# Kernel optimization log

Hardware: AMD Instinct MI355X
Metric: run time of the kernel (lower is better)

## Reference

```python
import jax, jax.numpy as jnp
import numpy as np

B, KVH, HPK, D = 4, 8, 4, 128          # batch, n_kv_heads, n_heads_per_kv, head_size
SEQ_KV = 4096                           # cached history length
SEQ = SEQ_KV + 1                        # history + current token
K, LOCAL_K, SINK, RANK = 512, 128, 4, 32


def gather(t, axis, i):
    """Broadcasting take_along_axis, mirroring the torch `gather` helper."""
    axis = axis % t.ndim
    tgt = list(t.shape)
    tgt[axis] = i.shape[axis]
    return jnp.take_along_axis(t, jnp.broadcast_to(i, tgt), axis)


def sparse_q_score(q, key_cpu_t, cur_key_t):
    # q: (B,KVH,HPK,1,D); key_cpu_t: (B,KVH,D,SEQ_KV); cur_key_t: (B,KVH,1,D,1)
    absq = jnp.abs(q).sum(2, keepdims=True)                    # (B,KVH,1,1,D)
    _, idx = jax.lax.top_k(absq, RANK)                         # (B,KVH,1,1,RANK)
    q_proj = gather(q, -1, idx)                                # (B,KVH,HPK,1,RANK)
    idx_t = jnp.swapaxes(idx, -1, -2)                          # (B,KVH,1,RANK,1)
    k_hist = gather(key_cpu_t[:, :, None], -2, idx_t)          # (B,KVH,1,RANK,SEQ_KV)
    k_cur = gather(cur_key_t, -2, idx_t)                       # (B,KVH,1,RANK,1)
    k_proj = jnp.concatenate([k_hist, k_cur], -1)              # (B,KVH,1,RANK,SEQ)
    scale = jnp.sqrt(jnp.abs(q_proj).sum(-1) / jnp.abs(q).sum(-1) * D)[..., None]
    return jnp.matmul(q_proj, k_proj) / scale                  # (B,KVH,HPK,1,SEQ)


def setup_inputs():
    key = jax.random.key(0)
    ks = jax.random.split(key, 6)
    query = jax.random.normal(ks[0], (B, KVH * HPK, 1, D), jnp.float32)
    k = jax.random.normal(ks[1], (B, KVH, 1, D), jnp.float32)
    v = jax.random.normal(ks[2], (B, KVH, 1, D), jnp.float32)
    logmask = jnp.zeros((B, KVH * HPK, 1, SEQ), jnp.float32)
    key_cpu = jax.random.normal(ks[3], (B, KVH, SEQ_KV, D), jnp.float32)
    value_cpu = jax.random.normal(ks[4], (B, KVH, SEQ_KV, D), jnp.float32)
    s_key_cpu = jnp.swapaxes(key_cpu, -1, -2)                  # head-size-contiguous copy
    mean_v = jax.random.normal(ks[5], (B, KVH, 1, 1, D), jnp.float32)
    return {"query": query, "key": k, "value": v, "logmask": logmask,
            "key_cpu": key_cpu, "value_cpu": value_cpu,
            "s_key_cpu": s_key_cpu, "mean_v": mean_v}


def reference(query, key, value, logmask, key_cpu, value_cpu, s_key_cpu, mean_v):
    q = query.reshape(B, KVH, HPK, 1, D)
    k = key.reshape(B, KVH, 1, 1, D)
    v = value.reshape(B, KVH, 1, 1, D)
    lm = logmask.reshape(B, KVH, HPK, 1, SEQ)
    # approximate scores over the full key history + current key
    score = (sparse_q_score(q, s_key_cpu, jnp.swapaxes(k, 3, 4)) + lm).astype(jnp.float32)
    # causal index over history (excluding current token): 0 = most recent unmasked
    neg = jnp.isneginf(lm[..., :-1])
    ci = jnp.where(neg, -1,
                   jnp.cumsum((~neg)[..., ::-1].astype(jnp.int32), -1)[..., ::-1] - 1)
    is_local = (0 <= ci) & (ci < LOCAL_K)
    is_sink = ci >= SEQ - SINK - 1
    fmax = jnp.finfo(jnp.float32).max
    topk_score = jnp.where(is_local | is_sink, fmax, score[..., :-1]).sum(2, keepdims=True)
    kk = min(K + SINK, SEQ)
    _, indices = jax.lax.top_k(topk_score, kk)                 # (B,KVH,1,1,kk)
    # running mean value update
    mean_v_new = (mean_v * (SEQ - 1) + v.astype(jnp.float32)) / SEQ
    # weight reallocation to the mean value
    norm = jax.nn.softmax(score, -1)
    kv_weight = gather(norm, -1, indices).sum(-1) + norm[..., -1]  # (B,KVH,HPK,1)
    # gather selected K/V and append current token
    kv_idx = indices[..., 0, :, None]                          # (B,KVH,1,kk,1)
    key_g = jnp.concatenate([gather(key_cpu[:, :, None], -2, kv_idx), k], -2)   # (B,KVH,1,kk+1,D)
    val_g = jnp.concatenate([gather(value_cpu[:, :, None], -2, kv_idx), v], -2)
    cur_idx = jnp.full(indices.shape[:-1] + (1,), SEQ - 1, indices.dtype)
    lm_g = gather(lm, -1, jnp.concatenate([indices, cur_idx], -1))  # (B,KVH,HPK,1,kk+1)
    # dense attention over the reduced key set
    scores = jnp.matmul(q, jnp.swapaxes(key_g, -1, -2)) * (D ** -0.5) + lm_g
    weights = jax.nn.softmax(scores.astype(jnp.float32), -1) * kv_weight[..., None]
    out = jnp.matmul(weights, val_g) + (1.0 - kv_weight[..., None]) * mean_v_new
    return out.reshape(B, KVH * HPK, 1, D), weights.reshape(B, KVH * HPK, 1, kk + 1)
```

## Files before the change

### kernel.cpp

```cpp
#include <hip/hip_runtime.h>
#include <hip/hip_bf16.h>
#include <math.h>

#define NBH 32
#define HPKN 4
#define DN 128
#define SEQKV 4096
#define SEQN 4097
#define SSTR 4100
#define RANKN 32
#define KSEL 516
#define SINKN 4
#define LOCALK 128
#define NMASK 132
#define NTOP 384
#define NCHUNK 16

__global__ __launch_bounds__(256) void k2_scores(
    const float* __restrict__ q, const float* __restrict__ key,
    const float* __restrict__ skey, const float* __restrict__ lm,
    float* __restrict__ scores, float* __restrict__ tk,
    float2* __restrict__ partials) {
  int bh = blockIdx.y;
  int s0 = blockIdx.x << 8;
  int t = threadIdx.x;
  int wave = t >> 6, lane = t & 63;
  __shared__ float qv[4][128];
  __shared__ float absq[128];
  __shared__ int sel[RANKN];
  __shared__ float qp[4][RANKN];
  __shared__ float wred[4][4];

  {
    float v0 = q[(size_t)bh * 512 + t];
    float v1 = q[(size_t)bh * 512 + 256 + t];
    qv[t >> 7][t & 127] = v0;
    qv[2 + (t >> 7)][t & 127] = v1;
  }
  __syncthreads();
  if (t < 128)
    absq[t] = fabsf(qv[0][t]) + fabsf(qv[1][t]) + fabsf(qv[2][t]) + fabsf(qv[3][t]);
  __syncthreads();
  if (t < 128) {
    float a = absq[t];
    int rank = 0;
    for (int e = 0; e < 128; ++e) {
      float ae = absq[e];
      rank += (ae > a) || (ae == a && e < t);
    }
    if (rank < RANKN) sel[rank] = t;
  }
  __syncthreads();
  {
    float fa = fabsf(qv[wave][lane]) + fabsf(qv[wave][lane + 64]);
    for (int off = 32; off > 0; off >>= 1) fa += __shfl_down(fa, off);
    float full = __shfl(fa, 0);
    float qsel = (lane < RANKN) ? qv[wave][sel[lane]] : 0.f;
    float sv = fabsf(qsel);
    for (int off = 32; off > 0; off >>= 1) sv += __shfl_down(sv, off);
    float selsum = __shfl(sv, 0);
    float scale = sqrtf(selsum / full * 128.f);
    if (lane < RANKN) qp[wave][lane] = qsel / scale;
  }
  __syncthreads();

  if (blockIdx.x == 0) {
    float kv = (lane < RANKN) ? key[bh * 128 + sel[lane]] : 0.f;
    float pr = (lane < RANKN) ? qp[wave][lane] * kv : 0.f;
    for (int off = 32; off > 0; off >>= 1) pr += __shfl_down(pr, off);
    if (lane == 0)
      scores[(size_t)(bh * 4 + wave) * SSTR + SEQKV] =
          pr + lm[(size_t)(bh * 4 + wave) * SEQN + SEQKV];
  }

  const float* kb = skey + (size_t)bh * 128 * 4096;
  float a0 = 0, a1 = 0, a2 = 0, a3 = 0;
#pragma unroll 8
  for (int r = 0; r < RANKN; ++r) {
    float k0 = kb[((size_t)sel[r] << 12) + s0 + t];
    a0 += qp[0][r] * k0;
    a1 += qp[1][r] * k0;
    a2 += qp[2][r] * k0;
    a3 += qp[3][r] * k0;
  }
  float sc[4];
  {
    int s = s0 + t;
    sc[0] = a0 + lm[(size_t)(bh * 4 + 0) * SEQN + s];
    sc[1] = a1 + lm[(size_t)(bh * 4 + 1) * SEQN + s];
    sc[2] = a2 + lm[(size_t)(bh * 4 + 2) * SEQN + s];
    sc[3] = a3 + lm[(size_t)(bh * 4 + 3) * SEQN + s];
    float sum = sc[0] + sc[1] + sc[2] + sc[3];
#pragma unroll
    for (int p = 0; p < 4; ++p)
      scores[(size_t)(bh * 4 + p) * SSTR + s] = sc[p];
    tk[(bh << 12) + s] = sum;
  }

#pragma unroll
  for (int p = 0; p < 4; ++p) {
    float mx = sc[p];
    for (int off = 32; off > 0; off >>= 1) mx = fmaxf(mx, __shfl_down(mx, off));
    if (lane == 0) wred[wave][p] = mx;
  }
  __syncthreads();
  float bm[4];
#pragma unroll
  for (int p = 0; p < 4; ++p)
    bm[p] = fmaxf(fmaxf(wred[0][p], wred[1][p]), fmaxf(wred[2][p], wred[3][p]));
  __syncthreads();
#pragma unroll
  for (int p = 0; p < 4; ++p) {
    float e = expf(sc[p] - bm[p]);
    for (int off = 32; off > 0; off >>= 1) e += __shfl_down(e, off);
    if (lane == 0) wred[wave][p] = e;
  }
  __syncthreads();
  if (t < 4) {
    float s = wred[0][t] + wred[1][t] + wred[2][t] + wred[3][t];
    partials[(size_t)(bh * 4 + t) * NCHUNK + blockIdx.x] = make_float2(bm[t], s);
  }
}

__global__ __launch_bounds__(256) void k3_topk(
    const float* __restrict__ tk, int* __restrict__ indices) {
  int bh = blockIdx.x;
  int t = threadIdx.x;
  int lane = t & 63;
  __shared__ unsigned us[4096];
  __shared__ unsigned hist[2048];
  __shared__ unsigned long long binlist[2048];
  __shared__ unsigned long long selk[512];
  __shared__ unsigned chunkSum[32];
  __shared__ int c1, c2, binB_s, nAbove_s, needed_s;

  {
    const float4* tk4 = (const float4*)(tk + (bh << 12));
    for (int i = t; i < 1024; i += 256) {
      float4 v = tk4[i];
      unsigned b0 = __float_as_uint(v.x), b1 = __float_as_uint(v.y);
      unsigned b2 = __float_as_uint(v.z), b3 = __float_as_uint(v.w);
      us[i * 4 + 0] = (b0 & 0x80000000u) ? ~b0 : (b0 | 0x80000000u);
      us[i * 4 + 1] = (b1 & 0x80000000u) ? ~b1 : (b1 | 0x80000000u);
      us[i * 4 + 2] = (b2 & 0x80000000u) ? ~b2 : (b2 | 0x80000000u);
      us[i * 4 + 3] = (b3 & 0x80000000u) ? ~b3 : (b3 | 0x80000000u);
    }
  }
  for (int i = t; i < 2048; i += 256) hist[i] = 0;
  if (t == 0) { c1 = 0; c2 = 0; }
  __syncthreads();

  for (int s = SINKN + t; s < SEQKV - LOCALK; s += 256)
    atomicAdd(&hist[us[s] >> 21], 1u);
  __syncthreads();

  if (t < 32) {
    unsigned sum = 0;
    for (int i = 0; i < 64; ++i) sum += hist[t * 64 + i];
    chunkSum[t] = sum;
  }
  __syncthreads();

  if (t < 64) {
    int l = t;
    unsigned x = (l < 32) ? chunkSum[l] : 0;
    unsigned sfx = x;
    for (int off = 1; off < 64; off <<= 1) {
      unsigned y = __shfl_down(sfx, off);
      if (l + off < 64) sfx += y;
    }
    unsigned above = sfx - x;
    bool hit = (l < 32) && (above < NTOP) && (above + x >= NTOP);
    unsigned long long mask = __ballot(hit);
    int C = __ffsll(mask) - 1;
    unsigned aboveC = __shfl(above, C);
    unsigned h = hist[C * 64 + l];
    unsigned sfx2 = h;
    for (int off = 1; off < 64; off <<= 1) {
      unsigned y = __shfl_down(sfx2, off);
      if (l + off < 64) sfx2 += y;
    }
    unsigned above2 = aboveC + (sfx2 - h);
    bool hit2 = (above2 < NTOP) && (above2 + h >= NTOP);
    unsigned long long mask2 = __ballot(hit2);
    int lB = __ffsll(mask2) - 1;
    if (l == lB) {
      binB_s = C * 64 + l;
      nAbove_s = (int)above2;
      needed_s = NTOP - (int)above2;
    }
  }
  __syncthreads();
  unsigned B = (unsigned)binB_s;
  int nAbove = nAbove_s, needed = needed_s;

  for (int s0 = SINKN; s0 < SEQKV - LOCALK; s0 += 256) {
    int s = s0 + t;
    bool valid = (s < SEQKV - LOCALK);
    unsigned u = valid ? us[s] : 0u;
    unsigned bin = u >> 21;
    bool win = valid && (bin > B);
    bool bnd = valid && (bin == B);
    unsigned long long mw = __ballot(win);
    unsigned long long mb = __ballot(bnd);
    int bw = 0, bb = 0;
    if (lane == 0) {
      if (mw) bw = atomicAdd(&c1, __popcll(mw));
      if (mb) bb = atomicAdd(&c2, __popcll(mb));
    }
    bw = __shfl(bw, 0);
    bb = __shfl(bb, 0);
    unsigned long long lmask = (1ULL << lane) - 1ULL;
    unsigned long long key = ((unsigned long long)u << 32) | (unsigned)(~s);
    if (win) selk[bw + __popcll(mw & lmask)] = key;
    if (bnd) {
      int pos = bb + __popcll(mb & lmask);
      if (pos < 2048) binlist[pos] = key;
    }
  }
  __syncthreads();
  int m2 = c2;
  int p2 = 1;
  while (p2 < m2) p2 <<= 1;
  for (int i = m2 + t; i < p2; i += 256) binlist[i] = 0ULL;
  __syncthreads();
  for (int k = 2; k <= p2; k <<= 1)
    for (int j = k >> 1; j > 0; j >>= 1) {
      for (int i = t; i < p2; i += 256) {
        int ixj = i ^ j;
        if (ixj > i) {
          bool desc = ((i & k) == 0);
          unsigned long long a = binlist[i], bb2 = binlist[ixj];
          if ((a < bb2) == desc) { binlist[i] = bb2; binlist[ixj] = a; }
        }
      }
      __syncthreads();
    }
  for (int i = t; i < needed; i += 256) selk[nAbove + i] = binlist[i];
  for (int i = NTOP + t; i < 512; i += 256) selk[i] = 0ULL;
  __syncthreads();

  unsigned long long e0 = selk[t], e1 = selk[t + 256];
  int i1 = t + 256;
  for (int k = 2; k <= 512; k <<= 1) {
    for (int j = k >> 1; j > 0; j >>= 1) {
      if (j == 256) {
        if (e0 < e1) { unsigned long long tmp = e0; e0 = e1; e1 = tmp; }
      } else if (j >= 64) {
        selk[t] = e0; selk[i1] = e1;
        __syncthreads();
        unsigned long long p0 = selk[t ^ j], p1 = selk[i1 ^ j];
        __syncthreads();
        bool d0 = ((t & k) == 0), l0 = ((t & j) == 0);
        e0 = (d0 == l0) ? (e0 > p0 ? e0 : p0) : (e0 < p0 ? e0 : p0);
        bool d1 = ((i1 & k) == 0), l1 = ((i1 & j) == 0);
        e1 = (d1 == l1) ? (e1 > p1 ? e1 : p1) : (e1 < p1 ? e1 : p1);
      } else {
        unsigned long long p0 = __shfl_xor(e0, j);
        unsigned long long p1 = __shfl_xor(e1, j);
        bool d0 = ((t & k) == 0), l0 = ((t & j) == 0);
        e0 = (d0 == l0) ? (e0 > p0 ? e0 : p0) : (e0 < p0 ? e0 : p0);
        bool d1 = ((i1 & k) == 0);
        e1 = (d1 == l0) ? (e1 > p1 ? e1 : p1) : (e1 < p1 ? e1 : p1);
      }
    }
  }

  if (t < SINKN) indices[bh * KSEL + t] = t;
  for (int i = t; i < LOCALK; i += 256)
    indices[bh * KSEL + SINKN + i] = (SEQKV - LOCALK) + i;
  indices[bh * KSEL + NMASK + t] = (int)(~(unsigned)(e0 & 0xFFFFFFFFu));
  if (t < NTOP - 256)
    indices[bh * KSEL + NMASK + 256 + t] = (int)(~(unsigned)(e1 & 0xFFFFFFFFu));
}

__global__ __launch_bounds__(256) void k5_qk(
    const float* __restrict__ q, const float* __restrict__ key,
    const float* __restrict__ lm, const float* __restrict__ key_cpu,
    const int* __restrict__ indices, float* __restrict__ s2_g) {
  int bh = blockIdx.y;
  int t = threadIdx.x;
  int wave = t >> 6, lane = t & 63;
  __shared__ float qs[512];
  __shared__ int sidx[KSEL];
  qs[t] = q[((size_t)bh * 4 << 7) + t];
  qs[t + 256] = q[((size_t)bh * 4 << 7) + t + 256];
  for (int j = t; j < KSEL; j += 256) sidx[j] = indices[bh * KSEL + j];
  __syncthreads();

  const float rsqd = 0.08838834764831845f;
  float q0a = qs[lane * 2], q0b = qs[lane * 2 + 1];
  float q1a = qs[128 + lane * 2], q1b = qs[128 + lane * 2 + 1];
  float q2a = qs[256 + lane * 2], q2b = qs[256 + lane * 2 + 1];
  float q3a = qs[384 + lane * 2], q3b = qs[384 + lane * 2 + 1];

  for (int i = 0; i < 5; ++i) {
    int j = (blockIdx.x << 2) + wave + 104 * i;
    if (j > KSEL) continue;
    int sj = (j < KSEL) ? sidx[j] : SEQKV;
    const float* krow = (j < KSEL)
        ? key_cpu + ((((size_t)bh << 12) + sj) << 7)
        : key + ((size_t)bh << 7);
    float2 kk = ((const float2*)krow)[lane];
    float p0 = q0a * kk.x + q0b * kk.y;
    float p1 = q1a * kk.x + q1b * kk.y;
    float p2 = q2a * kk.x + q2b * kk.y;
    float p3 = q3a * kk.x + q3b * kk.y;
    for (int off = 32; off > 0; off >>= 1) {
      p0 += __shfl_down(p0, off);
      p1 += __shfl_down(p1, off);
      p2 += __shfl_down(p2, off);
      p3 += __shfl_down(p3, off);
    }
    if (lane == 0) {
      size_t lmb = (size_t)bh * 4 * SEQN + sj;
      s2_g[(bh * 4 + 0) * 520 + j] = p0 * rsqd + lm[lmb + 0 * SEQN];
      s2_g[(bh * 4 + 1) * 520 + j] = p1 * rsqd + lm[lmb + 1 * SEQN];
      s2_g[(bh * 4 + 2) * 520 + j] = p2 * rsqd + lm[lmb + 2 * SEQN];
      s2_g[(bh * 4 + 3) * 520 + j] = p3 * rsqd + lm[lmb + 3 * SEQN];
    }
  }
}

__global__ __launch_bounds__(256) void k6_stats(
    const float* __restrict__ scores, const float2* __restrict__ partials,
    const int* __restrict__ indices, const float* __restrict__ s2_g,
    const float* __restrict__ value, const float* __restrict__ mean_v,
    float* __restrict__ out_w, float* __restrict__ w_g,
    float* __restrict__ out) {
  int bhp = blockIdx.x;
  int bh = bhp >> 2;
  int t = threadIdx.x;
  __shared__ int sidx[KSEL];
  __shared__ float red[256];
  __shared__ float bc;

  for (int j = t; j < KSEL; j += 256) sidx[j] = indices[bh * KSEL + j];
  __syncthreads();

  const float* srow = scores + (size_t)bhp * SSTR;
  float cur = srow[SEQKV];

  float m = cur, sumexp;
  {
    float2 pc[NCHUNK];
#pragma unroll
    for (int c = 0; c < NCHUNK; ++c) {
      pc[c] = partials[(size_t)bhp * NCHUNK + c];
      m = fmaxf(m, pc[c].x);
    }
    float s = expf(cur - m);
#pragma unroll
    for (int c = 0; c < NCHUNK; ++c) s += pc[c].y * expf(pc[c].x - m);
    sumexp = s;
  }

  float ss = 0.f;
  for (int j = t; j < KSEL; j += 256) ss += expf(srow[sidx[j]] - m);
  red[t] = ss; __syncthreads();
  for (int st = 128; st > 0; st >>= 1) {
    if (t < st) red[t] += red[t + st];
    __syncthreads();
  }
  float kvw;
  if (t == 0) bc = (red[0] + expf(cur - m)) / sumexp;
  __syncthreads();
  kvw = bc; __syncthreads();

  const float* s2r = s2_g + (size_t)bhp * 520;
  float mx2 = -INFINITY;
  for (int j = t; j < KSEL + 1; j += 256) mx2 = fmaxf(mx2, s2r[j]);
  red[t] = mx2; __syncthreads();
  for (int st = 128; st > 0; st >>= 1) {
    if (t < st) red[t] = fmaxf(red[t], red[t + st]);
    __syncthreads();
  }
  float m2 = red[0]; __syncthreads();
  float se2 = 0.f;
  for (int j = t; j < KSEL + 1; j += 256) se2 += expf(s2r[j] - m2);
  red[t] = se2; __syncthreads();
  for (int st = 128; st > 0; st >>= 1) {
    if (t < st) red[t] += red[t + st];
    __syncthreads();
  }
  float inv = kvw / red[0];

  for (int j = t; j < KSEL + 1; j += 256) {
    float w = expf(s2r[j] - m2) * inv;
    out_w[(size_t)bhp * (KSEL + 1) + j] = w;
    w_g[(size_t)bhp * 520 + j] = w;
  }

  if (t < 128) {
    float vcur = value[((size_t)bh << 7) + t];
    float mvn = (mean_v[((size_t)bh << 7) + t] * 4096.f + vcur) / 4097.f;
    out[((size_t)bhp << 7) + t] = (1.f - kvw) * mvn;
  }
}

__global__ __launch_bounds__(256) void k7_wv(
    const float* __restrict__ value, const float* __restrict__ value_cpu,
    const int* __restrict__ indices, const float* __restrict__ w_g,
    float* __restrict__ out) {
  int bh = blockIdx.y;
  int c0 = blockIdx.x << 5;
  int t = threadIdx.x;
  int d = t & 127, half = t >> 7;
  __shared__ int sidx[32];
  __shared__ float wsh[4][32];
  __shared__ float red[2][4][128];

  int nj = min(32, KSEL + 1 - c0);
  if (t < nj) {
    int j = c0 + t;
    sidx[t] = (j < KSEL) ? indices[bh * KSEL + j] : -1;
  }
  if (t < 128) {
    int p = t >> 5, jl = t & 31;
    wsh[p][jl] = (jl < nj) ? w_g[(size_t)(bh * 4 + p) * 520 + c0 + jl] : 0.f;
  }
  __syncthreads();

  float a0 = 0, a1 = 0, a2 = 0, a3 = 0;
  for (int jl = half; jl < nj; jl += 2) {
    int sj = sidx[jl];
    const float* vrow = (sj >= 0)
        ? value_cpu + ((((size_t)bh << 12) + sj) << 7)
        : value + ((size_t)bh << 7);
    float v = vrow[d];
    a0 += wsh[0][jl] * v;
    a1 += wsh[1][jl] * v;
    a2 += wsh[2][jl] * v;
    a3 += wsh[3][jl] * v;
  }
  red[half][0][d] = a0; red[half][1][d] = a1;
  red[half][2][d] = a2; red[half][3][d] = a3;
  __syncthreads();
  if (half == 0) {
#pragma unroll
    for (int p = 0; p < 4; ++p) {
      float s = red[0][p][d] + red[1][p][d];
      atomicAdd(&out[(size_t)(bh * 4 + p) * 128 + d], s);
    }
  }
}

extern "C" void kernel_launch(void* const* d_in, const int* in_sizes, int n_in,
                              void* d_out, int out_size, void* d_ws, size_t ws_size,
                              hipStream_t stream) {
  const float* query     = (const float*)d_in[0];
  const float* key       = (const float*)d_in[1];
  const float* value     = (const float*)d_in[2];
  const float* logmask   = (const float*)d_in[3];
  const float* key_cpu   = (const float*)d_in[4];
  const float* value_cpu = (const float*)d_in[5];
  const float* s_key_cpu = (const float*)d_in[6];
  const float* mean_v    = (const float*)d_in[7];

  float* out   = (float*)d_out;
  float* out_w = out + 16384;

  char* ws = (char*)d_ws;
  int*    indices  = (int*)(ws + 20480);
  float*  scores   = (float*)(ws + 86528);
  float*  tk       = (float*)(ws + 2185728);
  float*  s2_g     = (float*)(ws + 2710016);
  float*  w_g      = (float*)(ws + 2976256);
  float2* partials = (float2*)(ws + 3242496);

  hipLaunchKernelGGL(k2_scores, dim3(NCHUNK, NBH), dim3(256), 0, stream,
                     query, key, s_key_cpu, logmask, scores, tk, partials);
  hipLaunchKernelGGL(k3_topk, dim3(NBH), dim3(256), 0, stream,
                     tk, indices);
  hipLaunchKernelGGL(k5_qk, dim3(26, NBH), dim3(256), 0, stream,
                     query, key, logmask, key_cpu, indices, s2_g);
  hipLaunchKernelGGL(k6_stats, dim3(128), dim3(256), 0, stream,
                     scores, partials, indices, s2_g, value, mean_v,
                     out_w, w_g, out);
  hipLaunchKernelGGL(k7_wv, dim3(17, NBH), dim3(256), 0, stream,
                     value, value_cpu, indices, w_g, out);
}
```

Baseline: 229.2 us.

## Fuse five attention kernels into one cooperative kernel with grid syncs

Replaces the five separate launches (scores, top-k, qk, stats, wv) with a single cooperative kernel of 512 blocks that separates the phases with grid.sync(). The goal is to remove launch overhead and inter-kernel gaps, which matter at this small problem size. The cost is that only 32 of the 512 blocks do the top-k phase while the rest sit idle at the barrier, grid syncs have their own overhead, and the shared-memory union may limit occupancy.

After: 425.2 us. 85.5% more time.

```diff
diff --git a/kernel.cpp b/kernel.cpp
--- a/kernel.cpp
+++ b/kernel.cpp
@@ -1,6 +1,8 @@
 #include <hip/hip_runtime.h>
-#include <hip/hip_bf16.h>
+#include <hip/hip_cooperative_groups.h>
 #include <math.h>
+
+namespace cg = cooperative_groups;
 
 #define NBH 32
 #define HPKN 4
@@ -16,431 +18,434 @@
 #define NTOP 384
 #define NCHUNK 16
 
-__global__ __launch_bounds__(256) void k2_scores(
+__global__ __launch_bounds__(256, 2) void fused_all(
     const float* __restrict__ q, const float* __restrict__ key,
-    const float* __restrict__ skey, const float* __restrict__ lm,
+    const float* __restrict__ value, const float* __restrict__ lm,
+    const float* __restrict__ key_cpu, const float* __restrict__ value_cpu,
+    const float* __restrict__ skey, const float* __restrict__ mean_v,
     float* __restrict__ scores, float* __restrict__ tk,
-    float2* __restrict__ partials) {
-  int bh = blockIdx.y;
-  int s0 = blockIdx.x << 8;
-  int t = threadIdx.x;
-  int wave = t >> 6, lane = t & 63;
-  __shared__ float qv[4][128];
-  __shared__ float absq[128];
-  __shared__ int sel[RANKN];
-  __shared__ float qp[4][RANKN];
-  __shared__ float wred[4][4];
+    float2* __restrict__ partials, int* __restrict__ indices,
+    float* __restrict__ s2_g, float* __restrict__ w_g,
+    float* __restrict__ out, float* __restrict__ out_w) {
+  cg::grid_group grid = cg::this_grid();
+  const int bid = blockIdx.x;
+  const int bh = bid >> 4;
+  const int chunk = bid & 15;
+  const int t = threadIdx.x;
+  const int wave = t >> 6, lane = t & 63;
+
+  __shared__ __align__(16) char smem[45248];
+  __shared__ int c1, c2, binB_s, nAbove_s, needed_s;
+  __shared__ float bc6;
 
   {
-    float v0 = q[(size_t)bh * 512 + t];
-    float v1 = q[(size_t)bh * 512 + 256 + t];
-    qv[t >> 7][t & 127] = v0;
-    qv[2 + (t >> 7)][t & 127] = v1;
+    float* qv = (float*)smem;
+    float* absq = qv + 512;
+    int* sel = (int*)(absq + 128);
+    float* qp = (float*)(sel + 32);
+    float* wred = qp + 128;
+    const int s0 = chunk << 8;
+
+    {
+      float v0 = q[(size_t)bh * 512 + t];
+      float v1 = q[(size_t)bh * 512 + 256 + t];
+      qv[(t >> 7) * 128 + (t & 127)] = v0;
+      qv[(2 + (t >> 7)) * 128 + (t & 127)] = v1;
+    }
+    __syncthreads();
+    if (t < 128)
+      absq[t] = fabsf(qv[t]) + fabsf(qv[128 + t]) + fabsf(qv[256 + t]) +
+                fabsf(qv[384 + t]);
+    __syncthreads();
+    if (t < 128) {
+      float a = absq[t];
+      int rank = 0;
+      for (int e = 0; e < 128; ++e) {
+        float ae = absq[e];
+        rank += (ae > a) || (ae == a && e < t);
+      }
+      if (rank < RANKN) sel[rank] = t;
+    }
+    __syncthreads();
+    {
+      float fa = fabsf(qv[wave * 128 + lane]) + fabsf(qv[wave * 128 + lane + 64]);
+      for (int off = 32; off > 0; off >>= 1) fa += __shfl_down(fa, off);
+      float full = __shfl(fa, 0);
+      float qsel = (lane < RANKN) ? qv[wave * 128 + sel[lane]] : 0.f;
+      float sv = fabsf(qsel);
+      for (int off = 32; off > 0; off >>= 1) sv += __shfl_down(sv, off);
+      float selsum = __shfl(sv, 0);
+      float scale = sqrtf(selsum / full * 128.f);
+      if (lane < RANKN) qp[wave * RANKN + lane] = qsel / scale;
+    }
+    __syncthreads();
+
+    if (chunk == 0) {
+      float kv = (lane < RANKN) ? key[bh * 128 + sel[lane]] : 0.f;
+      float pr = (lane < RANKN) ? qp[wave * RANKN + lane] * kv : 0.f;
+      for (int off = 32; off > 0; off >>= 1) pr += __shfl_down(pr, off);
+      if (lane == 0)
+        scores[(size_t)(bh * 4 + wave) * SSTR + SEQKV] =
+            pr + lm[(size_t)(bh * 4 + wave) * SEQN + SEQKV];
+    }
+
+    const float* kb = skey + (size_t)bh * 128 * 4096;
+    float a0 = 0, a1 = 0, a2 = 0, a3 = 0;
+#pragma unroll 8
+    for (int r = 0; r < RANKN; ++r) {
+      float k0 = kb[((size_t)sel[r] << 12) + s0 + t];
+      a0 += qp[0 * RANKN + r] * k0;
+      a1 += qp[1 * RANKN + r] * k0;
+      a2 += qp[2 * RANKN + r] * k0;
+      a3 += qp[3 * RANKN + r] * k0;
+    }
+    float sc[4];
+    {
+      int s = s0 + t;
+      sc[0] = a0 + lm[(size_t)(bh * 4 + 0) * SEQN + s];
+      sc[1] = a1 + lm[(size_t)(bh * 4 + 1) * SEQN + s];
+      sc[2] = a2 + lm[(size_t)(bh * 4 + 2) * SEQN + s];
+      sc[3] = a3 + lm[(size_t)(bh * 4 + 3) * SEQN + s];
+      float sum = sc[0] + sc[1] + sc[2] + sc[3];
+#pragma unroll
+      for (int p = 0; p < 4; ++p)
+        scores[(size_t)(bh * 4 + p) * SSTR + s] = sc[p];
+      tk[(bh << 12) + s] = sum;
+    }
+
+#pragma unroll
+    for (int p = 0; p < 4; ++p) {
+      float mx = sc[p];
+      for (int off = 32; off > 0; off >>= 1) mx = fmaxf(mx, __shfl_down(mx, off));
+      if (lane == 0) wred[wave * 4 + p] = mx;
+    }
+    __syncthreads();
+    float bm[4];
+#pragma unroll
+    for (int p = 0; p < 4; ++p)
+      bm[p] = fmaxf(fmaxf(wred[0 * 4 + p], wred[1 * 4 + p]),
+                    fmaxf(wred[2 * 4 + p], wred[3 * 4 + p]));
+    __syncthreads();
+#pragma unroll
+    for (int p = 0; p < 4; ++p) {
+      float e = expf(sc[p] - bm[p]);
+      for (int off = 32; off > 0; off >>= 1) e += __shfl_down(e, off);
+      if (lane == 0) wred[wave * 4 + p] = e;
+    }
+    __syncthreads();
+    if (t < 4) {
+      float s = wred[0 * 4 + t] + wred[1 * 4 + t] + wred[2 * 4 + t] + wred[3 * 4 + t];
+      partials[(size_t)(bh * 4 + t) * NCHUNK + chunk] = make_float2(bm[t], s);
+    }
   }
-  __syncthreads();
-  if (t < 128)
-    absq[t] = fabsf(qv[0][t]) + fabsf(qv[1][t]) + fabsf(qv[2][t]) + fabsf(qv[3][t]);
-  __syncthreads();
-  if (t < 128) {
-    float a = absq[t];
-    int rank = 0;
-    for (int e = 0; e < 128; ++e) {
-      float ae = absq[e];
-      rank += (ae > a) || (ae == a && e < t);
-    }
-    if (rank < RANKN) sel[rank] = t;
+
+  grid.sync();
+
+  if (chunk == 0) {
+    unsigned* us = (unsigned*)smem;
+    unsigned* hist = us + 4096;
+    unsigned long long* binlist = (unsigned long long*)(hist + 2048);
+    unsigned long long* selk = binlist + 2048;
+    unsigned* chunkSum = (unsigned*)(selk + 512);
+
+    {
+      const float4* tk4 = (const float4*)(tk + (bh << 12));
+      for (int i = t; i < 1024; i += 256) {
+        float4 v = tk4[i];
+        unsigned b0 = __float_as_uint(v.x), b1 = __float_as_uint(v.y);
+        unsigned b2 = __float_as_uint(v.z), b3 = __float_as_uint(v.w);
+        us[i * 4 + 0] = (b0 & 0x80000000u) ? ~b0 : (b0 | 0x80000000u);
+        us[i * 4 + 1] = (b1 & 0x80000000u) ? ~b1 : (b1 | 0x80000000u);
+        us[i * 4 + 2] = (b2 & 0x80000000u) ? ~b2 : (b2 | 0x80000000u);
+        us[i * 4 + 3] = (b3 & 0x80000000u) ? ~b3 : (b3 | 0x80000000u);
+      }
+    }
+    for (int i = t; i < 2048; i += 256) hist[i] = 0;
+    if (t == 0) { c1 = 0; c2 = 0; }
+    __syncthreads();
+
+    for (int s = SINKN + t; s < SEQKV - LOCALK; s += 256)
+      atomicAdd(&hist[us[s] >> 21], 1u);
+    __syncthreads();
+
+    if (t < 32) {
+      unsigned sum = 0;
+      for (int i = 0; i < 64; ++i) sum += hist[t * 64 + i];
+      chunkSum[t] = sum;
+    }
+    __syncthreads();
+
+    if (t < 64) {
+      int l = t;
+      unsigned x = (l < 32) ? chunkSum[l] : 0;
+      unsigned sfx = x;
+      for (int off = 1; off < 64; off <<= 1) {
+        unsigned y = __shfl_down(sfx, off);
+        if (l + off < 64) sfx += y;
+      }
+      unsigned above = sfx - x;
+      bool hit = (l < 32) && (above < NTOP) && (above + x >= NTOP);
+      unsigned long long mask = __ballot(hit);
+      int C = __ffsll(mask) - 1;
+      unsigned aboveC = __shfl(above, C);
+      unsigned h = hist[C * 64 + l];
+      unsigned sfx2 = h;
+      for (int off = 1; off < 64; off <<= 1) {
+        unsigned y = __shfl_down(sfx2, off);
+        if (l + off < 64) sfx2 += y;
+      }
+      unsigned above2 = aboveC + (sfx2 - h);
+      bool hit2 = (above2 < NTOP) && (above2 + h >= NTOP);
+      unsigned long long mask2 = __ballot(hit2);
+      int lB = __ffsll(mask2) - 1;
+      if (l == lB) {
+        binB_s = C * 64 + l;
+        nAbove_s = (int)above2;
+        needed_s = NTOP - (int)above2;
+      }
+    }
+    __syncthreads();
+    unsigned binB = (unsigned)binB_s;
+    int nAbove = nAbove_s, needed = needed_s;
+
+    for (int s0 = SINKN; s0 < SEQKV - LOCALK; s0 += 256) {
+      int s = s0 + t;
+      bool valid = (s < SEQKV - LOCALK);
+      unsigned u = valid ? us[s] : 0u;
+      unsigned bin = u >> 21;
+      bool win = valid && (bin > binB);
+      bool bnd = valid && (bin == binB);
+      unsigned long long mw = __ballot(win);
+      unsigned long long mb = __ballot(bnd);
+      int bw = 0, bb = 0;
+      if (lane == 0) {
+        if (mw) bw = atomicAdd(&c1, __popcll(mw));
+        if (mb) bb = atomicAdd(&c2, __popcll(mb));
+      }
+      bw = __shfl(bw, 0);
+      bb = __shfl(bb, 0);
+      unsigned long long lmask = (1ULL << lane) - 1ULL;
+      unsigned long long keyv = ((unsigned long long)u << 32) | (unsigned)(~s);
+      if (win) selk[bw + __popcll(mw & lmask)] = keyv;
+      if (bnd) {
+        int pos = bb + __popcll(mb & lmask);
+        if (pos < 2048) binlist[pos] = keyv;
+      }
+    }
+    __syncthreads();
+    int m2 = c2;
+    int p2 = 1;
+    while (p2 < m2) p2 <<= 1;
+    for (int i = m2 + t; i < p2; i += 256) binlist[i] = 0ULL;
+    __syncthreads();
+    for (int k = 2; k <= p2; k <<= 1)
+      for (int j = k >> 1; j > 0; j >>= 1) {
+        for (int i = t; i < p2; i += 256) {
+          int ixj = i ^ j;
+          if (ixj > i) {
+            bool desc = ((i & k) == 0);
+            unsigned long long a = binlist[i], bb2 = binlist[ixj];
+            if ((a < bb2) == desc) { binlist[i] = bb2; binlist[ixj] = a; }
+          }
+        }
+        __syncthreads();
+      }
+    for (int i = t; i < needed; i += 256) selk[nAbove + i] = binlist[i];
+    for (int i = NTOP + t; i < 512; i += 256) selk[i] = 0ULL;
+    __syncthreads();
+
+    unsigned long long e0 = selk[t], e1 = selk[t + 256];
+    int i1 = t + 256;
+    for (int k = 2; k <= 512; k <<= 1) {
+      for (int j = k >> 1; j > 0; j >>= 1) {
+        if (j == 256) {
+          if (e0 < e1) { unsigned long long tmp = e0; e0 = e1; e1 = tmp; }
+        } else if (j >= 64) {
+          selk[t] = e0; selk[i1] = e1;
+          __syncthreads();
+          unsigned long long p0 = selk[t ^ j], p1 = selk[i1 ^ j];
+          __syncthreads();
+          bool d0 = ((t & k) == 0), l0 = ((t & j) == 0);
+          e0 = (d0 == l0) ? (e0 > p0 ? e0 : p0) : (e0 < p0 ? e0 : p0);
+          bool d1 = ((i1 & k) == 0), l1 = ((i1 & j) == 0);
+          e1 = (d1 == l1) ? (e1 > p1 ? e1 : p1) : (e1 < p1 ? e1 : p1);
+        } else {
+          unsigned long long p0 = __shfl_xor(e0, j);
+          unsigned long long p1 = __shfl_xor(e1, j);
+          bool d0 = ((t & k) == 0), l0 = ((t & j) == 0);
+          e0 = (d0 == l0) ? (e0 > p0 ? e0 : p0) : (e0 < p0 ? e0 : p0);
+          bool d1 = ((i1 & k) == 0);
+          e1 = (d1 == l0) ? (e1 > p1 ? e1 : p1) : (e1 < p1 ? e1 : p1);
+        }
+      }
+    }
+
+    if (t < SINKN) indices[bh * KSEL + t] = t;
+    for (int i = t; i < LOCALK; i += 256)
+      indices[bh * KSEL + SINKN + i] = (SEQKV - LOCALK) + i;
+    indices[bh * KSEL + NMASK + t] = (int)(~(unsigned)(e0 & 0xFFFFFFFFu));
+    if (t < NTOP - 256)
+      indices[bh * KSEL + NMASK + 256 + t] = (int)(~(unsigned)(e1 & 0xFFFFFFFFu));
   }
-  __syncthreads();
+
+  grid.sync();
+
   {
-    float fa = fabsf(qv[wave][lane]) + fabsf(qv[wave][lane + 64]);
-    for (int off = 32; off > 0; off >>= 1) fa += __shfl_down(fa, off);
-    float full = __shfl(fa, 0);
-    float qsel = (lane < RANKN) ? qv[wave][sel[lane]] : 0.f;
-    float sv = fabsf(qsel);
-    for (int off = 32; off > 0; off >>= 1) sv += __shfl_down(sv, off);
-    float selsum = __shfl(sv, 0);
-    float scale = sqrtf(selsum / full * 128.f);
-    if (lane < RANKN) qp[wave][lane] = qsel / scale;
+    float* qs = (float*)smem;
+    int* sidx = (int*)(qs + 512);
+    qs[t] = q[((size_t)bh << 9) + t];
+    qs[t + 256] = q[((size_t)bh << 9) + t + 256];
+    for (int j = t; j < KSEL; j += 256) sidx[j] = indices[bh * KSEL + j];
+    __syncthreads();
+
+    const float rsqd = 0.08838834764831845f;
+    float q0a = qs[lane * 2], q0b = qs[lane * 2 + 1];
+    float q1a = qs[128 + lane * 2], q1b = qs[128 + lane * 2 + 1];
+    float q2a = qs[256 + lane * 2], q2b = qs[256 + lane * 2 + 1];
+    float q3a = qs[384 + lane * 2], q3b = qs[384 + lane * 2 + 1];
+
+    for (int m = wave; m < 33; m += 4) {
+      int j = chunk + (m << 4);
+      if (j > KSEL) continue;
+      int sj = (j < KSEL) ? sidx[j] : SEQKV;
+      const float* krow = (j < KSEL)
+          ? key_cpu + ((((size_t)bh << 12) + sj) << 7)
+          : key + ((size_t)bh << 7);
+      float2 kk = ((const float2*)krow)[lane];
+      float p0 = q0a * kk.x + q0b * kk.y;
+      float p1 = q1a * kk.x + q1b * kk.y;
+      float p2 = q2a * kk.x + q2b * kk.y;
+      float p3 = q3a * kk.x + q3b * kk.y;
+      for (int off = 32; off > 0; off >>= 1) {
+        p0 += __shfl_down(p0, off);
+        p1 += __shfl_down(p1, off);
+        p2 += __shfl_down(p2, off);
+        p3 += __shfl_down(p3, off);
+      }
+      if (lane == 0) {
+        size_t lmb = (size_t)bh * 4 * SEQN + sj;
+        s2_g[(bh * 4 + 0) * 520 + j] = p0 * rsqd + lm[lmb + 0 * SEQN];
+        s2_g[(bh * 4 + 1) * 520 + j] = p1 * rsqd + lm[lmb + 1 * SEQN];
+        s2_g[(bh * 4 + 2) * 520 + j] = p2 * rsqd + lm[lmb + 2 * SEQN];
+        s2_g[(bh * 4 + 3) * 520 + j] = p3 * rsqd + lm[lmb + 3 * SEQN];
+      }
+    }
   }
-  __syncthreads();
-
-  if (blockIdx.x == 0) {
-    float kv = (lane < RANKN) ? key[bh * 128 + sel[lane]] : 0.f;
-    float pr = (lane < RANKN) ? qp[wave][lane] * kv : 0.f;
-    for (int off = 32; off > 0; off >>= 1) pr += __shfl_down(pr, off);
-    if (lane == 0)
-      scores[(size_t)(bh * 4 + wave) * SSTR + SEQKV] =
-          pr + lm[(size_t)(bh * 4 + wave) * SEQN + SEQKV];
+
+  grid.sync();
+
+  if (bid < 128) {
+    const int bhp = bid;
+    const int bh4 = bhp >> 2;
+    int* sidx = (int*)smem;
+    float* red = (float*)(sidx + 520);
+
+    for (int j = t; j < KSEL; j += 256) sidx[j] = indices[bh4 * KSEL + j];
+    __syncthreads();
+
+    const float* srow = scores + (size_t)bhp * SSTR;
+    float cur = srow[SEQKV];
+
+    float m = cur, sumexp;
+    {
+      float2 pc[NCHUNK];
+#pragma unroll
+      for (int c = 0; c < NCHUNK; ++c) {
+        pc[c] = partials[(size_t)bhp * NCHUNK + c];
+        m = fmaxf(m, pc[c].x);
+      }
+      float s = expf(cur - m);
+#pragma unroll
+      for (int c = 0; c < NCHUNK; ++c) s += pc[c].y * expf(pc[c].x - m);
+      sumexp = s;
+    }
+
+    float ss = 0.f;
+    for (int j = t; j < KSEL; j += 256) ss += expf(srow[sidx[j]] - m);
+    red[t] = ss; __syncthreads();
+    for (int st = 128; st > 0; st >>= 1) {
+      if (t < st) red[t] += red[t + st];
+      __syncthreads();
+    }
+    if (t == 0) bc6 = (red[0] + expf(cur - m)) / sumexp;
+    __syncthreads();
+    float kvw = bc6; __syncthreads();
+
+    const float* s2r = s2_g + (size_t)bhp * 520;
+    float mx2 = -INFINITY;
+    for (int j = t; j < KSEL + 1; j += 256) mx2 = fmaxf(mx2, s2r[j]);
+    red[t] = mx2; __syncthreads();
+    for (int st = 128; st > 0; st >>= 1) {
+      if (t < st) red[t] = fmaxf(red[t], red[t + st]);
+      __syncthreads();
+    }
+    float m2 = red[0]; __syncthreads();
+    float se2 = 0.f;
+    for (int j = t; j < KSEL + 1; j += 256) se2 += expf(s2r[j] - m2);
+    red[t] = se2; __syncthreads();
+    for (int st = 128; st > 0; st >>= 1) {
+      if (t < st) red[t] += red[t + st];
+      __syncthreads();
+    }
+    float inv = kvw / red[0];
+
+    for (int j = t; j < KSEL + 1; j += 256) {
+      float w = expf(s2r[j] - m2) * inv;
+      out_w[(size_t)bhp * (KSEL + 1) + j] = w;
+      w_g[(size_t)bhp * 520 + j] = w;
+    }
+
+    if (t < 128) {
+      float vcur = value[((size_t)bh4 << 7) + t];
+      float mvn = (mean_v[((size_t)bh4 << 7) + t] * 4096.f + vcur) / 4097.f;
+      out[((size_t)bhp << 7) + t] = (1.f - kvw) * mvn;
+    }
   }
 
-  const float* kb = skey + (size_t)bh * 128 * 4096;
-  float a0 = 0, a1 = 0, a2 = 0, a3 = 0;
-#pragma unroll 8
-  for (int r = 0; r < RANKN; ++r) {
-    float k0 = kb[((size_t)sel[r] << 12) + s0 + t];
-    a0 += qp[0][r] * k0;
-    a1 += qp[1][r] * k0;
-    a2 += qp[2][r] * k0;
-    a3 += qp[3][r] * k0;
-  }
-  float sc[4];
+  grid.sync();
+
   {
-    int s = s0 + t;
-    sc[0] = a0 + lm[(size_t)(bh * 4 + 0) * SEQN + s];
-    sc[1] = a1 + lm[(size_t)(bh * 4 + 1) * SEQN + s];
-    sc[2] = a2 + lm[(size_t)(bh * 4 + 2) * SEQN + s];
-    sc[3] = a3 + lm[(size_t)(bh * 4 + 3) * SEQN + s];
-    float sum = sc[0] + sc[1] + sc[2] + sc[3];
-#pragma unroll
-    for (int p = 0; p < 4; ++p)
-      scores[(size_t)(bh * 4 + p) * SSTR + s] = sc[p];
-    tk[(bh << 12) + s] = sum;
-  }
-
-#pragma unroll
-  for (int p = 0; p < 4; ++p) {
-    float mx = sc[p];
-    for (int off = 32; off > 0; off >>= 1) mx = fmaxf(mx, __shfl_down(mx, off));
-    if (lane == 0) wred[wave][p] = mx;
-  }
-  __syncthreads();
-  float bm[4];
-#pragma unroll
-  for (int p = 0; p < 4; ++p)
-    bm[p] = fmaxf(fmaxf(wred[0][p], wred[1][p]), fmaxf(wred[2][p], wred[3][p]));
-  __syncthreads();
-#pragma unroll
-  for (int p = 0; p < 4; ++p) {
-    float e = expf(sc[p] - bm[p]);
-    for (int off = 32; off > 0; off >>= 1) e += __shfl_down(e, off);
-    if (lane == 0) wred[wave][p] = e;
-  }
-  __syncthreads();
-  if (t < 4) {
-    float s = wred[0][t] + wred[1][t] + wred[2][t] + wred[3][t];
-    partials[(size_t)(bh * 4 + t) * NCHUNK + blockIdx.x] = make_float2(bm[t], s);
-  }
-}
-
-__global__ __launch_bounds__(256) void k3_topk(
-    const float* __restrict__ tk, int* __restrict__ indices) {
-  int bh = blockIdx.x;
-  int t = threadIdx.x;
-  int lane = t & 63;
-  __shared__ unsigned us[4096];
-  __shared__ unsigned hist[2048];
-  __shared__ unsigned long long binlist[2048];
-  __shared__ unsigned long long selk[512];
-  __shared__ unsigned chunkSum[32];
-  __shared__ int c1, c2, binB_s, nAbove_s, needed_s;
-
-  {
-    const float4* tk4 = (const float4*)(tk + (bh << 12));
-    for (int i = t; i < 1024; i += 256) {
-      float4 v = tk4[i];
-      unsigned b0 = __float_as_uint(v.x), b1 = __float_as_uint(v.y);
-      unsigned b2 = __float_as_uint(v.z), b3 = __float_as_uint(v.w);
-      us[i * 4 + 0] = (b0 & 0x80000000u) ? ~b0 : (b0 | 0x80000000u);
-      us[i * 4 + 1] = (b1 & 0x80000000u) ? ~b1 : (b1 | 0x80000000u);
-      us[i * 4 + 2] = (b2 & 0x80000000u) ? ~b2 : (b2 | 0x80000000u);
-      us[i * 4 + 3] = (b3 & 0x80000000u) ? ~b3 : (b3 | 0x80000000u);
-    }
-  }
-  for (int i = t; i < 2048; i += 256) hist[i] = 0;
-  if (t == 0) { c1 = 0; c2 = 0; }
-  __syncthreads();
-
-  for (int s = SINKN + t; s < SEQKV - LOCALK; s += 256)
-    atomicAdd(&hist[us[s] >> 21], 1u);
-  __syncthreads();
-
-  if (t < 32) {
-    unsigned sum = 0;
-    for (int i = 0; i < 64; ++i) sum += hist[t * 64 + i];
-    chunkSum[t] = sum;
-  }
-  __syncthreads();
-
-  if (t < 64) {
-    int l = t;
-    unsigned x = (l < 32) ? chunkSum[l] : 0;
-    unsigned sfx = x;
-    for (int off = 1; off < 64; off <<= 1) {
-      unsigned y = __shfl_down(sfx, off);
-      if (l + off < 64) sfx += y;
-    }
-    unsigned above = sfx - x;
-    bool hit = (l < 32) && (above < NTOP) && (above + x >= NTOP);
-    unsigned long long mask = __ballot(hit);
-    int C = __ffsll(mask) - 1;
-    unsigned aboveC = __shfl(above, C);
-    unsigned h = hist[C * 64 + l];
-    unsigned sfx2 = h;
-    for (int off = 1; off < 64; off <<= 1) {
-      unsigned y = __shfl_down(sfx2, off);
-      if (l + off < 64) sfx2 += y;
-    }
-    unsigned above2 = aboveC + (sfx2 - h);
-    bool hit2 = (above2 < NTOP) && (above2 + h >= NTOP);
-    unsigned long long mask2 = __ballot(hit2);
-    int lB = __ffsll(mask2) - 1;
-    if (l == lB) {
-      binB_s = C * 64 + l;
-      nAbove_s = (int)above2;
-      needed_s = NTOP - (int)above2;
-    }
-  }
-  __syncthreads();
-  unsigned B = (unsigned)binB_s;
-  int nAbove = nAbove_s, needed = needed_s;
-
-  for (int s0 = SINKN; s0 < SEQKV - LOCALK; s0 += 256) {
-    int s = s0 + t;
-    bool valid = (s < SEQKV - LOCALK);
-    unsigned u = valid ? us[s] : 0u;
-    unsigned bin = u >> 21;
-    bool win = valid && (bin > B);
-    bool bnd = valid && (bin == B);
-    unsigned long long mw = __ballot(win);
-    unsigned long long mb = __ballot(bnd);
-    int bw = 0, bb = 0;
-    if (lane == 0) {
-      if (mw) bw = atomicAdd(&c1, __popcll(mw));
-      if (mb) bb = atomicAdd(&c2, __popcll(mb));
-    }
-    bw = __shfl(bw, 0);
-    bb = __shfl(bb, 0);
-    unsigned long long lmask = (1ULL << lane) - 1ULL;
-    unsigned long long key = ((unsigned long long)u << 32) | (unsigned)(~s);
-    if (win) selk[bw + __popcll(mw & lmask)] = key;
-    if (bnd) {
-      int pos = bb + __popcll(mb & lmask);
-      if (pos < 2048) binlist[pos] = key;
-    }
-  }
-  __syncthreads();
-  int m2 = c2;
-  int p2 = 1;
-  while (p2 < m2) p2 <<= 1;
-  for (int i = m2 + t; i < p2; i += 256) binlist[i] = 0ULL;
-  __syncthreads();
-  for (int k = 2; k <= p2; k <<= 1)
-    for (int j = k >> 1; j > 0; j >>= 1) {
-      for (int i = t; i < p2; i += 256) {
-        int ixj = i ^ j;
-        if (ixj > i) {
-          bool desc = ((i & k) == 0);
-          unsigned long long a = binlist[i], bb2 = binlist[ixj];
-          if ((a < bb2) == desc) { binlist[i] = bb2; binlist[ixj] = a; }
-        }
-      }
-      __syncthreads();
-    }
-  for (int i = t; i < needed; i += 256) selk[nAbove + i] = binlist[i];
-  for (int i = NTOP + t; i < 512; i += 256) selk[i] = 0ULL;
-  __syncthreads();
-
-  unsigned long long e0 = selk[t], e1 = selk[t + 256];
-  int i1 = t + 256;
-  for (int k = 2; k <= 512; k <<= 1) {
-    for (int j = k >> 1; j > 0; j >>= 1) {
-      if (j == 256) {
-        if (e0 < e1) { unsigned long long tmp = e0; e0 = e1; e1 = tmp; }
-      } else if (j >= 64) {
-        selk[t] = e0; selk[i1] = e1;
-        __syncthreads();
-        unsigned long long p0 = selk[t ^ j], p1 = selk[i1 ^ j];
-        __syncthreads();
-        bool d0 = ((t & k) == 0), l0 = ((t & j) == 0);
-        e0 = (d0 == l0) ? (e0 > p0 ? e0 : p0) : (e0 < p0 ? e0 : p0);
-        bool d1 = ((i1 & k) == 0), l1 = ((i1 & j) == 0);
-        e1 = (d1 == l1) ? (e1 > p1 ? e1 : p1) : (e1 < p1 ? e1 : p1);
-      } else {
-        unsigned long long p0 = __shfl_xor(e0, j);
-        unsigned long long p1 = __shfl_xor(e1, j);
-        bool d0 = ((t & k) == 0), l0 = ((t & j) == 0);
-        e0 = (d0 == l0) ? (e0 > p0 ? e0 : p0) : (e0 < p0 ? e0 : p0);
-        bool d1 = ((i1 & k) == 0);
-        e1 = (d1 == l0) ? (e1 > p1 ? e1 : p1) : (e1 < p1 ? e1 : p1);
-      }
-    }
-  }
-
-  if (t < SINKN) indices[bh * KSEL + t] = t;
-  for (int i = t; i < LOCALK; i += 256)
-    indices[bh * KSEL + SINKN + i] = (SEQKV - LOCALK) + i;
-  indices[bh * KSEL + NMASK + t] = (int)(~(unsigned)(e0 & 0xFFFFFFFFu));
-  if (t < NTOP - 256)
-    indices[bh * KSEL + NMASK + 256 + t] = (int)(~(unsigned)(e1 & 0xFFFFFFFFu));
-}
-
-__global__ __launch_bounds__(256) void k5_qk(
-    const float* __restrict__ q, const float* __restrict__ key,
-    const float* __restrict__ lm, const float* __restrict__ key_cpu,
-    const int* __restrict__ indices, float* __restrict__ s2_g) {
-  int bh = blockIdx.y;
-  int t = threadIdx.x;
-  int wave = t >> 6, lane = t & 63;
-  __shared__ float qs[512];
-  __shared__ int sidx[KSEL];
-  qs[t] = q[((size_t)bh * 4 << 7) + t];
-  qs[t + 256] = q[((size_t)bh * 4 << 7) + t + 256];
-  for (int j = t; j < KSEL; j += 256) sidx[j] = indices[bh * KSEL + j];
-  __syncthreads();
-
-  const float rsqd = 0.08838834764831845f;
-  float q0a = qs[lane * 2], q0b = qs[lane * 2 + 1];
-  float q1a = qs[128 + lane * 2], q1b = qs[128 + lane * 2 + 1];
-  float q2a = qs[256 + lane * 2], q2b = qs[256 + lane * 2 + 1];
-  float q3a = qs[384 + lane * 2], q3b = qs[384 + lane * 2 + 1];
-
-  for (int i = 0; i < 5; ++i) {
-    int j = (blockIdx.x << 2) + wave + 104 * i;
-    if (j > KSEL) continue;
-    int sj = (j < KSEL) ? sidx[j] : SEQKV;
-    const float* krow = (j < KSEL)
-        ? key_cpu + ((((size_t)bh << 12) + sj) << 7)
-        : key + ((size_t)bh << 7);
-    float2 kk = ((const float2*)krow)[lane];
-    float p0 = q0a * kk.x + q0b * kk.y;
-    float p1 = q1a * kk.x + q1b * kk.y;
-    float p2 = q2a * kk.x + q2b * kk.y;
-    float p3 = q3a * kk.x + q3b * kk.y;
-    for (int off = 32; off > 0; off >>= 1) {
-      p0 += __shfl_down(p0, off);
-      p1 += __shfl_down(p1, off);
-      p2 += __shfl_down(p2, off);
-      p3 += __shfl_down(p3, off);
-    }
-    if (lane == 0) {
-      size_t lmb = (size_t)bh * 4 * SEQN + sj;
-      s2_g[(bh * 4 + 0) * 520 + j] = p0 * rsqd + lm[lmb + 0 * SEQN];
-      s2_g[(bh * 4 + 1) * 520 + j] = p1 * rsqd + lm[lmb + 1 * SEQN];
-      s2_g[(bh * 4 + 2) * 520 + j] = p2 * rsqd + lm[lmb + 2 * SEQN];
-      s2_g[(bh * 4 + 3) * 520 + j] = p3 * rsqd + lm[lmb + 3 * SEQN];
-    }
-  }
-}
-
-__global__ __launch_bounds__(256) void k6_stats(
-    const float* __restrict__ scores, const float2* __restrict__ partials,
-    const int* __restrict__ indices, const float* __restrict__ s2_g,
-    const float* __restrict__ value, const float* __restrict__ mean_v,
-    float* __restrict__ out_w, float* __restrict__ w_g,
-    float* __restrict__ out) {
-  int bhp = blockIdx.x;
-  int bh = bhp >> 2;
-  int t = threadIdx.x;
-  __shared__ int sidx[KSEL];
-  __shared__ float red[256];
-  __shared__ float bc;
-
-  for (int j = t; j < KSEL; j += 256) sidx[j] = indices[bh * KSEL + j];
-  __syncthreads();
-
-  const float* srow = scores + (size_t)bhp * SSTR;
-  float cur = srow[SEQKV];
-
-  float m = cur, sumexp;
-  {
-    float2 pc[NCHUNK];
-#pragma unroll
-    for (int c = 0; c < NCHUNK; ++c) {
-      pc[c] = partials[(size_t)bhp * NCHUNK + c];
-      m = fmaxf(m, pc[c].x);
-    }
-    float s = expf(cur - m);
-#pragma unroll
-    for (int c = 0; c < NCHUNK; ++c) s += pc[c].y * expf(pc[c].x - m);
-    sumexp = s;
-  }
-
-  float ss = 0.f;
-  for (int j = t; j < KSEL; j += 256) ss += expf(srow[sidx[j]] - m);
-  red[t] = ss; __syncthreads();
-  for (int st = 128; st > 0; st >>= 1) {
-    if (t < st) red[t] += red[t + st];
-    __syncthreads();
-  }
-  float kvw;
-  if (t == 0) bc = (red[0] + expf(cur - m)) / sumexp;
-  __syncthreads();
-  kvw = bc; __syncthreads();
-
-  const float* s2r = s2_g + (size_t)bhp * 520;
-  float mx2 = -INFINITY;
-  for (int j = t; j < KSEL + 1; j += 256) mx2 = fmaxf(mx2, s2r[j]);
-  red[t] = mx2; __syncthreads();
-  for (int st = 128; st > 0; st >>= 1) {
-    if (t < st) red[t] = fmaxf(red[t], red[t + st]);
-    __syncthreads();
-  }
-  float m2 = red[0]; __syncthreads();
-  float se2 = 0.f;
-  for (int j = t; j < KSEL + 1; j += 256) se2 += expf(s2r[j] - m2);
-  red[t] = se2; __syncthreads();
-  for (int st = 128; st > 0; st >>= 1) {
-    if (t < st) red[t] += red[t + st];
-    __syncthreads();
-  }
-  float inv = kvw / red[0];
-
-  for (int j = t; j < KSEL + 1; j += 256) {
-    float w = expf(s2r[j] - m2) * inv;
-    out_w[(size_t)bhp * (KSEL + 1) + j] = w;
-    w_g[(size_t)bhp * 520 + j] = w;
-  }
-
-  if (t < 128) {
-    float vcur = value[((size_t)bh << 7) + t];
-    float mvn = (mean_v[((size_t)bh << 7) + t] * 4096.f + vcur) / 4097.f;
-    out[((size_t)bhp << 7) + t] = (1.f - kvw) * mvn;
-  }
-}
-
-__global__ __launch_bounds__(256) void k7_wv(
-    const float* __restrict__ value, const float* __restrict__ value_cpu,
-    const int* __restrict__ indices, const float* __restrict__ w_g,
-    float* __restrict__ out) {
-  int bh = blockIdx.y;
-  int c0 = blockIdx.x << 5;
-  int t = threadIdx.x;
-  int d = t & 127, half = t >> 7;
-  __shared__ int sidx[32];
-  __shared__ float wsh[4][32];
-  __shared__ float red[2][4][128];
-
-  int nj = min(32, KSEL + 1 - c0);
-  if (t < nj) {
-    int j = c0 + t;
-    sidx[t] = (j < KSEL) ? indices[bh * KSEL + j] : -1;
-  }
-  if (t < 128) {
-    int p = t >> 5, jl = t & 31;
-    wsh[p][jl] = (jl < nj) ? w_g[(size_t)(bh * 4 + p) * 520 + c0 + jl] : 0.f;
-  }
-  __syncthreads();
-
-  float a0 = 0, a1 = 0, a2 = 0, a3 = 0;
-  for (int jl = half; jl < nj; jl += 2) {
-    int sj = sidx[jl];
-    const float* vrow = (sj >= 0)
-        ? value_cpu + ((((size_t)bh << 12) + sj) << 7)
-        : value + ((size_t)bh << 7);
-    float v = vrow[d];
-    a0 += wsh[0][jl] * v;
-    a1 += wsh[1][jl] * v;
-    a2 += wsh[2][jl] * v;
-    a3 += wsh[3][jl] * v;
-  }
-  red[half][0][d] = a0; red[half][1][d] = a1;
-  red[half][2][d] = a2; red[half][3][d] = a3;
-  __syncthreads();
-  if (half == 0) {
-#pragma unroll
-    for (int p = 0; p < 4; ++p) {
-      float s = red[0][p][d] + red[1][p][d];
-      atomicAdd(&out[(size_t)(bh * 4 + p) * 128 + d], s);
+    const int c0 = chunk * 33;
+    const int nj = min(33, KSEL + 1 - c0);
+    const int d = t & 127, half = t >> 7;
+    int* sidx = (int*)smem;
+    float* wsh = (float*)(sidx + 36);
+    float* red = wsh + 136;
+
+    if (t < nj) {
+      int j = c0 + t;
+      sidx[t] = (j < KSEL) ? indices[bh * KSEL + j] : -1;
+    }
+    if (t < 33) {
+#pragma unroll
+      for (int p = 0; p < 4; ++p)
+        wsh[p * 33 + t] = (t < nj) ? w_g[(size_t)(bh * 4 + p) * 520 + c0 + t] : 0.f;
+    }
+    __syncthreads();
+
+    float a0 = 0, a1 = 0, a2 = 0, a3 = 0;
+    for (int jl = half; jl < nj; jl += 2) {
+      int sj = sidx[jl];
+      const float* vrow = (sj >= 0)
+          ? value_cpu + ((((size_t)bh << 12) + sj) << 7)
+          : value + ((size_t)bh << 7);
+      float v = vrow[d];
+      a0 += wsh[0 * 33 + jl] * v;
+      a1 += wsh[1 * 33 + jl] * v;
+      a2 += wsh[2 * 33 + jl] * v;
+      a3 += wsh[3 * 33 + jl] * v;
+    }
+    red[(half * 4 + 0) * 128 + d] = a0;
+    red[(half * 4 + 1) * 128 + d] = a1;
+    red[(half * 4 + 2) * 128 + d] = a2;
+    red[(half * 4 + 3) * 128 + d] = a3;
+    __syncthreads();
+    if (half == 0) {
+#pragma unroll
+      for (int p = 0; p < 4; ++p) {
+        float s = red[(0 * 4 + p) * 128 + d] + red[(1 * 4 + p) * 128 + d];
+        atomicAdd(&out[(size_t)(bh * 4 + p) * 128 + d], s);
+      }
     }
   }
 }
@@ -468,15 +473,11 @@
   float*  w_g      = (float*)(ws + 2976256);
   float2* partials = (float2*)(ws + 3242496);
 
-  hipLaunchKernelGGL(k2_scores, dim3(NCHUNK, NBH), dim3(256), 0, stream,
-                     query, key, s_key_cpu, logmask, scores, tk, partials);
-  hipLaunchKernelGGL(k3_topk, dim3(NBH), dim3(256), 0, stream,
-                     tk, indices);
-  hipLaunchKernelGGL(k5_qk, dim3(26, NBH), dim3(256), 0, stream,
-                     query, key, logmask, key_cpu, indices, s2_g);
-  hipLaunchKernelGGL(k6_stats, dim3(128), dim3(256), 0, stream,
-                     scores, partials, indices, s2_g, value, mean_v,
-                     out_w, w_g, out);
-  hipLaunchKernelGGL(k7_wv, dim3(17, NBH), dim3(256), 0, stream,
-                     value, value_cpu, indices, w_g, out);
+  void* args[] = {
+      (void*)&query, (void*)&key, (void*)&value, (void*)&logmask,
+      (void*)&key_cpu, (void*)&value_cpu, (void*)&s_key_cpu, (void*)&mean_v,
+      (void*)&scores, (void*)&tk, (void*)&partials, (void*)&indices,
+      (void*)&s2_g, (void*)&w_g, (void*)&out, (void*)&out_w};
+  hipLaunchCooperativeKernel((void*)fused_all, dim3(512), dim3(256), args, 0,
+                             stream);
 }
```
